# Performance work log

Measured on AMD Instinct MI355X. Metric: run time of the kernel, lower is better.

Reference implementation:

```python
import jax, jax.numpy as jnp
import numpy as np

DIM = 1024
HEADS = 16
DIM_HEAD = 64
SOFTCAP = 50.0


def setup_inputs() -> dict:
    key = jax.random.key(0)
    k1, k2, k3, k4 = jax.random.split(key, 4)
    b, n = 2, 2048
    dim_inner = HEADS * DIM_HEAD
    x = jax.random.normal(k1, (b, n, DIM), dtype=jnp.float32)
    # parameters stored as math-orientation matrices (in_features, out_features)
    w_qkv = jax.random.normal(k2, (DIM, 3 * dim_inner), dtype=jnp.float32) * 0.02
    w_gates = jax.random.normal(k3, (DIM, HEADS), dtype=jnp.float32) * 0.02
    w_out = jax.random.normal(k4, (dim_inner, DIM), dtype=jnp.float32) * 0.02
    return {"x": x, "w_qkv": w_qkv, "w_gates": w_gates, "w_out": w_out}


def reference(x, w_qkv, w_gates, w_out):
    b, n, _ = x.shape
    scale = DIM_HEAD ** -0.5
    qkv = jnp.einsum('bnf,fe->bne', x, w_qkv).reshape(b, n, 3, HEADS, DIM_HEAD)
    qkv = jnp.moveaxis(qkv, 2, 0)            # 3 b n h d
    q, k, v = jnp.moveaxis(qkv, 3, 2)         # each: b h n d
    q = q * scale
    sim = jnp.einsum('bhid,bhjd->bhij', q, k)
    # tanh softcap on raw scores
    sim = SOFTCAP * jnp.tanh(sim / SOFTCAP)
    # causal mask (prefill path, causal=True)
    mask_value = -jnp.finfo(sim.dtype).max
    causal_mask = jnp.triu(jnp.ones((n, n), dtype=bool), 1)
    sim = jnp.where(causal_mask, mask_value, sim)
    attn = jax.nn.softmax(sim, axis=-1)
    out = jnp.einsum('bhij,bhjd->bhid', attn, v)
    # value gating: sigmoid(x @ Wg) -> b h n 1
    gates = jax.nn.sigmoid(jnp.einsum('bnf,fh->bhn', x, w_gates))[..., None]
    out = out * gates
    # b h n d -> b n (h d) -> output projection
    out = jnp.transpose(out, (0, 2, 1, 3)).reshape(b, n, HEADS * DIM_HEAD)
    return jnp.einsum('bne,ef->bnf', out, w_out)
```

## Files before the change

kernel.cpp:

```cpp
#include <hip/hip_runtime.h>
#include <hip/hip_bf16.h>

typedef __bf16 bf16x8 __attribute__((ext_vector_type(8)));
typedef float f32x4 __attribute__((ext_vector_type(4)));

__device__ __forceinline__ unsigned short f2b(float f) {
    union { float f; unsigned int u; } v; v.f = f;
    unsigned int r = (v.u + 0x7FFFu + ((v.u >> 16) & 1u)) >> 16;
    return (unsigned short)r;
}

__device__ __forceinline__ unsigned int cvtpk(float lo, float hi) {
    unsigned int r;
    asm("v_cvt_pk_bf16_f32 %0, %1, %2" : "=v"(r) : "v"(lo), "v"(hi));
    return r;
}

__device__ __forceinline__ void gload_lds16(const void* g, void* l) {
    __builtin_amdgcn_global_load_lds((__attribute__((address_space(1))) void*)g,
                                     (__attribute__((address_space(3))) void*)l,
                                     16, 0, 0);
}


__global__ __launch_bounds__(256)
void prepass_kernel(const float* __restrict__ x, const float* __restrict__ wg,
                    const float* __restrict__ wq, const float* __restrict__ wo,
                    unsigned short* __restrict__ xb, float* __restrict__ gates,
                    unsigned short* __restrict__ outq, unsigned short* __restrict__ outo) {
    __shared__ float xs[1024];
    __shared__ float red[16][17];
    __shared__ float tt[32][33];
    const int t = threadIdx.x;
    if (blockIdx.x < 4096) {
        const int row = blockIdx.x;
        const float* xr = x + (size_t)row * 1024;
        float4 f = *(const float4*)(xr + t * 4);
        *(float4*)(xs + t * 4) = f;
        ushort4 u;
        u.x = f2b(f.x); u.y = f2b(f.y); u.z = f2b(f.z); u.w = f2b(f.w);
        *(ushort4*)(xb + (size_t)row * 1024 + t * 4) = u;
        __syncthreads();
        const int h = t & 15, fi = t >> 4;
        float s = 0.f;
        for (int ff = fi; ff < 1024; ff += 16)
            s += xs[ff] * wg[ff * 16 + h];
        red[fi][h] = s;
        __syncthreads();
        if (t < 16) {
            float tot = 0.f;
#pragma unroll
            for (int i = 0; i < 16; i++) tot += red[i][t];
            int b = row >> 11, n = row & 2047;
            gates[((size_t)(b * 16 + t)) * 2048 + n] = 1.f / (1.f + __expf(-tot));
        }
    } else {
        const int bx = blockIdx.x - 4096;
        const int colTile = bx & 127;
        const int r0 = (bx >> 7) * 32;
        const float* in;
        unsigned short* out;
        int C, c0;
        if (colTile < 96) { in = wq; out = outq; C = 3072; c0 = colTile * 32; }
        else              { in = wo; out = outo; C = 1024; c0 = (colTile - 96) * 32; }
        const int tx = t & 31, ty = t >> 5;
#pragma unroll
        for (int i = 0; i < 4; i++)
            tt[ty + i * 8][tx] = in[(size_t)(r0 + ty + i * 8) * C + c0 + tx];
        __syncthreads();
#pragma unroll
        for (int i = 0; i < 4; i++)
            out[(size_t)(c0 + ty + i * 8) * 1024 + r0 + tx] = f2b(tt[tx][ty + i * 8]);
    }
}


template <int EPI, int WN>
__global__ __launch_bounds__(256)
void gemm_bt_kernel(const unsigned short* __restrict__ A,
                    const unsigned short* __restrict__ Bt,
                    int M, int N, int K,
                    unsigned short* __restrict__ outQ,
                    unsigned short* __restrict__ outK,
                    unsigned short* __restrict__ outV,
                    float* __restrict__ outF) {
    constexpr int WM = 4 / WN;
    constexpr int MF = 8 / WM;
    constexpr int BN = 64 * WN;
    __shared__ unsigned short As[2][128 * 32];
    __shared__ unsigned short Bs[2][BN * 32];
    const int lane = threadIdx.x & 63;
    const int w = threadIdx.x >> 6;
    const int wr = w / WN, wc = w % WN;
    const int tm = blockIdx.y * 128;
    const int tn = blockIdx.x * BN;

    f32x4 acc[MF][4];
#pragma unroll
    for (int m = 0; m < MF; m++)
#pragma unroll
        for (int n = 0; n < 4; n++) acc[m][n] = (f32x4){0.f, 0.f, 0.f, 0.f};

    const int sRow = lane >> 2;
    const int sCol = (lane & 3) * 8;
    const int fragA = (wr * (16 * MF) + (lane & 15)) * 32 + (lane >> 4) * 8;
    const int fragB = (wc * 64 + (lane & 15)) * 32 + (lane >> 4) * 8;

    auto STAGE = [&](int k0, int buf) {
#pragma unroll
        for (int i = 0; i < 2; i++) {
            int chunk = w * 2 + i;
            int r = chunk * 16 + sRow;
            gload_lds16(A + (size_t)(tm + r) * K + k0 + sCol, (void*)(As[buf] + chunk * 512));
            if (WN == 2)
                gload_lds16(Bt + (size_t)(tn + r) * K + k0 + sCol, (void*)(Bs[buf] + chunk * 512));
        }
        if (WN == 1) {
            int r = w * 16 + sRow;
            gload_lds16(Bt + (size_t)(tn + r) * K + k0 + sCol, (void*)(Bs[buf] + w * 512));
        }
    };

    STAGE(0, 0);
    __syncthreads();
    int cur = 0;
    for (int k0 = 0; k0 < K; k0 += 32) {
        if (k0 + 32 < K) STAGE(k0 + 32, cur ^ 1);
        bf16x8 af[MF], bg[4];
#pragma unroll
        for (int m = 0; m < MF; m++) af[m] = *(const bf16x8*)(As[cur] + fragA + m * 16 * 32);
#pragma unroll
        for (int n = 0; n < 4; n++) bg[n] = *(const bf16x8*)(Bs[cur] + fragB + n * 16 * 32);
#pragma unroll
        for (int m = 0; m < MF; m++)
#pragma unroll
            for (int n = 0; n < 4; n++)
                acc[m][n] = __builtin_amdgcn_mfma_f32_16x16x32_bf16(af[m], bg[n], acc[m][n], 0, 0, 0);
        __syncthreads();
        cur ^= 1;
    }

#pragma unroll
    for (int m = 0; m < MF; m++) {
        int row = tm + wr * (16 * MF) + m * 16 + (lane >> 4) * 4;
#pragma unroll
        for (int n = 0; n < 4; n++) {
            int col = tn + wc * 64 + n * 16 + (lane & 15);
            if (EPI == 0) {
                int which = col >> 10;
                int hh = (col >> 6) & 15;
                int d = col & 63;
                int b0 = row >> 11;
                int nn = row & 2047;
                size_t bh = (size_t)(b0 * 16 + hh);
                if (which == 2) {
                    int i6 = nn & 63;
                    int pc = (nn & ~63) + ((i6 >> 2) & 3) * 16 + ((i6 >> 4) & 3) * 4;
                    ushort4 st;
                    st.x = f2b(acc[m][n][0]);
                    st.y = f2b(acc[m][n][1]);
                    st.z = f2b(acc[m][n][2]);
                    st.w = f2b(acc[m][n][3]);
                    *(ushort4*)(outV + bh * 131072 + (size_t)d * 2048 + pc) = st;
                } else if (which == 0) {
                    size_t off = (bh * 2048 + nn) * 64 + d;
#pragma unroll
                    for (int r = 0; r < 4; r++)
                        outQ[off + (size_t)r * 64] = f2b(acc[m][n][r] * 0.125f);
                } else {
                    size_t off = (bh * 2048 + nn) * 64 + d;
#pragma unroll
                    for (int r = 0; r < 4; r++)
                        outK[off + (size_t)r * 64] = f2b(acc[m][n][r]);
                }
            } else {
#pragma unroll
                for (int r = 0; r < 4; r++)
                    outF[(size_t)(row + r) * N + col] = acc[m][n][r];
            }
        }
    }
}


__global__ __launch_bounds__(256)
void attn_kernel(const unsigned short* __restrict__ Q,
                 const unsigned short* __restrict__ Kg,
                 const unsigned short* __restrict__ Vp,
                 const float* __restrict__ Gates,
                 unsigned short* __restrict__ Out) {
    __shared__ unsigned short lds[2][2][2][64][64];

    const int lane = threadIdx.x & 63;
    const int w = threadIdx.x >> 6;
    const int g = lane >> 4;
    const int ql = lane & 15;
    const int sw = ql & 7;
    const int srow = lane >> 3;
    const int sch = lane & 7;

    const int wgid = (blockIdx.x & 7) * 64 + (blockIdx.x >> 3);
    const int bh = wgid >> 4;
    const int pair = wgid & 15;
    const int b = bh >> 4;
    const int h = bh & 15;

    const size_t headBase = (size_t)bh * 2048 * 64;
    const size_t vBase = (size_t)bh * 131072;

    const int koff0 = ((g) ^ sw) * 8;
    const int koff1 = ((g + 4) ^ sw) * 8;
    const int voff0 = ((2 * g) ^ sw) * 8;
    const int voff1 = ((2 * g + 1) ^ sw) * 8;

    const int ch = sch ^ srow;
    const unsigned short* kSt0 = Kg + headBase + (size_t)(w * 16 + srow) * 64 + ch * 8;
    const unsigned short* kSt1 = kSt0 + 8 * 64;
    const unsigned short* vSt0 = Vp + vBase + (size_t)(w * 16 + srow) * 2048 + ch * 8;
    const unsigned short* vSt1 = vSt0 + 8 * 2048;

    auto STAGE = [&](int jn, int buf, int slot) {
        gload_lds16(kSt0 + (size_t)jn * 4096, (void*)&lds[buf][slot][0][w * 16][0]);
        gload_lds16(kSt1 + (size_t)jn * 4096, (void*)&lds[buf][slot][0][w * 16 + 8][0]);
        gload_lds16(vSt0 + jn * 64, (void*)&lds[buf][slot][1][w * 16][0]);
        gload_lds16(vSt1 + jn * 64, (void*)&lds[buf][slot][1][w * 16 + 8][0]);
    };

    const float LOG2E = 1.4426950408889634f;
    const float LC1 = -1.9235933878519511e-4f;
    const float LC2 = 3.0777494205631219e-8f;

    for (int half = 0; half < 2; half++) {
        const int qt = half ? (31 - pair) : pair;
        const int qglob = qt * 64 + w * 16 + ql;
        const int T = qt + 1;
        const int nPairs = (T + 1) >> 1;

        const unsigned short* qp = Q + headBase + (size_t)qglob * 64 + g * 8;
        bf16x8 qa0 = *(const bf16x8*)qp;
        bf16x8 qa1 = *(const bf16x8*)(qp + 32);

        float lsum = 0.f;
        f32x4 o[4];
#pragma unroll
        for (int n = 0; n < 4; n++) o[n] = (f32x4){0.f, 0.f, 0.f, 0.f};

        auto COMPUTE = [&](int jt, int bb, int slot, bool diag) {
            const unsigned short* KL = &lds[bb][slot][0][0][0];
            const unsigned short* VL = &lds[bb][slot][1][0][0];

            f32x4 s4[4];
            __builtin_amdgcn_s_setprio(1);
#pragma unroll
            for (int n = 0; n < 4; n++) {
                const unsigned short* kr = KL + (16 * n + ql) * 64;
                bf16x8 k0 = *(const bf16x8*)(kr + koff0);
                bf16x8 k1 = *(const bf16x8*)(kr + koff1);
                f32x4 sv = (f32x4){0.f, 0.f, 0.f, 0.f};
                sv = __builtin_amdgcn_mfma_f32_16x16x32_bf16(k0, qa0, sv, 0, 0, 0);
                sv = __builtin_amdgcn_mfma_f32_16x16x32_bf16(k1, qa1, sv, 0, 0, 0);
                s4[n] = sv;
            }
            __builtin_amdgcn_s_setprio(0);

            float rs = 0.f;
#pragma unroll
            for (int n = 0; n < 4; n++) {
                int k0c = jt * 64 + n * 16 + 4 * g;
#pragma unroll
                for (int r = 0; r < 4; r++) {
                    float xx = s4[n][r];
                    float x2 = xx * xx;
                    float e2 = xx * __builtin_fmaf(x2, __builtin_fmaf(x2, LC2, LC1), LOG2E);
                    if (diag && (k0c + r > qglob)) e2 = -1e30f;
                    float p = __builtin_amdgcn_exp2f(e2);
                    s4[n][r] = p;
                    rs += p;
                }
            }
            lsum += rs;

            union PU { unsigned int u[4]; bf16x8 v; };
            PU p0, p1;
            p0.u[0] = cvtpk(s4[0][0], s4[0][1]);
            p0.u[1] = cvtpk(s4[0][2], s4[0][3]);
            p0.u[2] = cvtpk(s4[1][0], s4[1][1]);
            p0.u[3] = cvtpk(s4[1][2], s4[1][3]);
            p1.u[0] = cvtpk(s4[2][0], s4[2][1]);
            p1.u[1] = cvtpk(s4[2][2], s4[2][3]);
            p1.u[2] = cvtpk(s4[3][0], s4[3][1]);
            p1.u[3] = cvtpk(s4[3][2], s4[3][3]);

            __builtin_amdgcn_s_setprio(1);
#pragma unroll
            for (int n = 0; n < 4; n++) {
                const unsigned short* vr = VL + (16 * n + ql) * 64;
                bf16x8 vA = *(const bf16x8*)(vr + voff0);
                bf16x8 vB = *(const bf16x8*)(vr + voff1);
                o[n] = __builtin_amdgcn_mfma_f32_16x16x32_bf16(vA, p0.v, o[n], 0, 0, 0);
                o[n] = __builtin_amdgcn_mfma_f32_16x16x32_bf16(vB, p1.v, o[n], 0, 0, 0);
            }
            __builtin_amdgcn_s_setprio(0);
        };

        STAGE(0, 0, 0);
        if (1 <= qt) STAGE(1, 0, 1);
        __syncthreads();

        for (int p = 0; p < nPairs - 1; ++p) {
            const int bb = p & 1;
            const int j2 = 2 * (p + 1);
            STAGE(j2, bb ^ 1, 0);
            if (j2 + 1 <= qt) STAGE(j2 + 1, bb ^ 1, 1);
            COMPUTE(2 * p, bb, 0, false);
            COMPUTE(2 * p + 1, bb, 1, false);
            __syncthreads();
        }
        {
            const int p = nPairs - 1;
            const int bb = p & 1;
            COMPUTE(2 * p, bb, 0, 2 * p == qt);
            if (2 * p + 1 <= qt) COMPUTE(2 * p + 1, bb, 1, true);
            __syncthreads();
        }

        float l = lsum;
        l += __shfl_xor(l, 16);
        l += __shfl_xor(l, 32);
        float gate = Gates[(size_t)bh * 2048 + qglob];
        float inv = gate / l;
        unsigned short* orow = Out + ((size_t)(b * 2048) + qglob) * 1024 + h * 64;
#pragma unroll
        for (int n = 0; n < 4; n++) {
            ushort4 st;
            st.x = f2b(o[n][0] * inv);
            st.y = f2b(o[n][1] * inv);
            st.z = f2b(o[n][2] * inv);
            st.w = f2b(o[n][3] * inv);
            *(ushort4*)(orow + n * 16 + 4 * g) = st;
        }
    }
}


extern "C" void kernel_launch(void* const* d_in, const int* in_sizes, int n_in,
                              void* d_out, int out_size, void* d_ws, size_t ws_size,
                              hipStream_t stream) {
    const float* x       = (const float*)d_in[0];
    const float* w_qkv   = (const float*)d_in[1];
    const float* w_gates = (const float*)d_in[2];
    const float* w_out   = (const float*)d_in[3];
    float* out = (float*)d_out;

    char* ws = (char*)d_ws;
    unsigned short* x_bf  = (unsigned short*)(ws);
    unsigned short* wqkvT = (unsigned short*)(ws + ((size_t)8  << 20));
    unsigned short* woutT = (unsigned short*)(ws + ((size_t)14 << 20));
    unsigned short* qB    = (unsigned short*)(ws + ((size_t)16 << 20));
    unsigned short* kB    = (unsigned short*)(ws + ((size_t)24 << 20));
    unsigned short* vP    = (unsigned short*)(ws + ((size_t)32 << 20));
    float*          gates = (float*)(ws + ((size_t)40 << 20));
    unsigned short* attnO = (unsigned short*)(ws + ((size_t)41 << 20));

    prepass_kernel<<<dim3(8192), dim3(256), 0, stream>>>(
        x, w_gates, w_qkv, w_out, x_bf, gates, wqkvT, woutT);

    gemm_bt_kernel<0, 2><<<dim3(3072 / 128, 4096 / 128), dim3(256), 0, stream>>>(
        x_bf, wqkvT, 4096, 3072, 1024, qB, kB, vP, (float*)nullptr);

    attn_kernel<<<dim3(512), dim3(256), 0, stream>>>(qB, kB, vP, gates, attnO);

    gemm_bt_kernel<1, 1><<<dim3(1024 / 64, 4096 / 128), dim3(256), 0, stream>>>(
        attnO, woutT, 4096, 1024, 1024, nullptr, nullptr, nullptr, out);
}
```

Measured before the change: 127.1 us.

## Move gate projection from scalar prepass to separate bf16 MFMA kernel

The prepass no longer computes the sigmoid gates with a per-row scalar dot product and LDS reduction. It now only converts x to bf16 with wider vectorized blocks and also writes a transposed bf16 copy of w_gates. A new small kernel computes the gate projection with 16x16x32 bf16 MFMA instructions, split over four waves along K, then applies a fast exp2/rcp sigmoid. This adds one kernel launch and rounds the gate inputs to bf16, in exchange for removing the slow scalar gate loop from the prepass.

```diff
diff --git a/kernel.cpp b/kernel.cpp
--- a/kernel.cpp
+++ b/kernel.cpp
@@ -26,36 +26,22 @@
 __global__ __launch_bounds__(256)
 void prepass_kernel(const float* __restrict__ x, const float* __restrict__ wg,
                     const float* __restrict__ wq, const float* __restrict__ wo,
-                    unsigned short* __restrict__ xb, float* __restrict__ gates,
-                    unsigned short* __restrict__ outq, unsigned short* __restrict__ outo) {
-    __shared__ float xs[1024];
-    __shared__ float red[16][17];
+                    unsigned short* __restrict__ xb,
+                    unsigned short* __restrict__ outq, unsigned short* __restrict__ outo,
+                    unsigned short* __restrict__ wgT) {
     __shared__ float tt[32][33];
     const int t = threadIdx.x;
-    if (blockIdx.x < 4096) {
-        const int row = blockIdx.x;
-        const float* xr = x + (size_t)row * 1024;
-        float4 f = *(const float4*)(xr + t * 4);
-        *(float4*)(xs + t * 4) = f;
-        ushort4 u;
-        u.x = f2b(f.x); u.y = f2b(f.y); u.z = f2b(f.z); u.w = f2b(f.w);
-        *(ushort4*)(xb + (size_t)row * 1024 + t * 4) = u;
-        __syncthreads();
-        const int h = t & 15, fi = t >> 4;
-        float s = 0.f;
-        for (int ff = fi; ff < 1024; ff += 16)
-            s += xs[ff] * wg[ff * 16 + h];
-        red[fi][h] = s;
-        __syncthreads();
-        if (t < 16) {
-            float tot = 0.f;
-#pragma unroll
-            for (int i = 0; i < 16; i++) tot += red[i][t];
-            int b = row >> 11, n = row & 2047;
-            gates[((size_t)(b * 16 + t)) * 2048 + n] = 1.f / (1.f + __expf(-tot));
-        }
-    } else {
-        const int bx = blockIdx.x - 4096;
+    if (blockIdx.x < 2048) {
+        size_t idx = ((size_t)blockIdx.x * 256 + t) * 8;
+        float4 f0 = *(const float4*)(x + idx);
+        float4 f1 = *(const float4*)(x + idx + 4);
+        ushort4 u0, u1;
+        u0.x = f2b(f0.x); u0.y = f2b(f0.y); u0.z = f2b(f0.z); u0.w = f2b(f0.w);
+        u1.x = f2b(f1.x); u1.y = f2b(f1.y); u1.z = f2b(f1.z); u1.w = f2b(f1.w);
+        *(ushort4*)(xb + idx) = u0;
+        *(ushort4*)(xb + idx + 4) = u1;
+    } else if (blockIdx.x < 6144) {
+        const int bx = blockIdx.x - 2048;
         const int colTile = bx & 127;
         const int r0 = (bx >> 7) * 32;
         const float* in;
@@ -71,6 +57,50 @@
 #pragma unroll
         for (int i = 0; i < 4; i++)
             out[(size_t)(c0 + ty + i * 8) * 1024 + r0 + tx] = f2b(tt[tx][ty + i * 8]);
+    } else {
+        const int local = blockIdx.x - 6144;
+        const int base = local * 4096 + t * 16;
+        const int f = base >> 4;
+#pragma unroll
+        for (int j = 0; j < 16; j++)
+            wgT[j * 1024 + f] = f2b(wg[base + j]);
+    }
+}
+
+
+__global__ __launch_bounds__(256)
+void gates_mfma_kernel(const unsigned short* __restrict__ xb,
+                       const unsigned short* __restrict__ wgT,
+                       float* __restrict__ gates) {
+    __shared__ float comb[4][16][16];
+    const int lane = threadIdx.x & 63;
+    const int w = threadIdx.x >> 6;
+    const int ql = lane & 15;
+    const int g = lane >> 4;
+    const int n0 = blockIdx.x * 16;
+
+    f32x4 acc = (f32x4){0.f, 0.f, 0.f, 0.f};
+    const int kb = w * 256;
+#pragma unroll
+    for (int kk = 0; kk < 256; kk += 32) {
+        bf16x8 a = *(const bf16x8*)(wgT + ql * 1024 + kb + kk + g * 8);
+        bf16x8 bfr = *(const bf16x8*)(xb + (size_t)(n0 + ql) * 1024 + kb + kk + g * 8);
+        acc = __builtin_amdgcn_mfma_f32_16x16x32_bf16(a, bfr, acc, 0, 0, 0);
+    }
+#pragma unroll
+    for (int r = 0; r < 4; r++) comb[w][g * 4 + r][ql] = acc[r];
+    __syncthreads();
+    if (w == 0) {
+        const float LOG2E = 1.4426950408889634f;
+        int row = n0 + ql;
+        int b = row >> 11, n = row & 2047;
+#pragma unroll
+        for (int r = 0; r < 4; r++) {
+            int h = g * 4 + r;
+            float tot = comb[0][h][ql] + comb[1][h][ql] + comb[2][h][ql] + comb[3][h][ql];
+            float sg = __builtin_amdgcn_rcpf(1.f + __builtin_amdgcn_exp2f(-tot * LOG2E));
+            gates[((size_t)(b * 16 + h)) * 2048 + n] = sg;
+        }
     }
 }
 
@@ -360,10 +390,13 @@
     unsigned short* kB    = (unsigned short*)(ws + ((size_t)24 << 20));
     unsigned short* vP    = (unsigned short*)(ws + ((size_t)32 << 20));
     float*          gates = (float*)(ws + ((size_t)40 << 20));
+    unsigned short* wgT   = (unsigned short*)(ws + ((size_t)40 << 20) + (512 << 10));
     unsigned short* attnO = (unsigned short*)(ws + ((size_t)41 << 20));
 
-    prepass_kernel<<<dim3(8192), dim3(256), 0, stream>>>(
-        x, w_gates, w_qkv, w_out, x_bf, gates, wqkvT, woutT);
+    prepass_kernel<<<dim3(6148), dim3(256), 0, stream>>>(
+        x, w_gates, w_qkv, w_out, x_bf, wqkvT, woutT, wgT);
+
+    gates_mfma_kernel<<<dim3(256), dim3(256), 0, stream>>>(x_bf, wgT, gates);
 
     gemm_bt_kernel<0, 2><<<dim3(3072 / 128, 4096 / 128), dim3(256), 0, stream>>>(
         x_bf, wqkvT, 4096, 3072, 1024, qB, kB, vP, (float*)nullptr);
```

New measurement: 109.5 us, median of 2. -13.8%, faster.
